# Optimization experiments

Measured on AMD Instinct MI355X. Metric: run time of the kernel, lower is better.

## Reference

```python
import jax, jax.numpy as jnp
import numpy as np

B, S, H = 2, 2048, 2048
NH, NKV, HD = 16, 4, 128
SCALING = HD ** -0.5


def rotate_half(x):
    x1, x2 = jnp.split(x, 2, axis=-1)
    return jnp.concatenate((-x2, x1), axis=-1)


def apply_rope(t, cos, sin):
    # t: [B, nh, S, HD]; cos/sin: [B, S, HD] -> unsqueeze head dim
    c = cos[:, None, :, :]
    s = sin[:, None, :, :]
    return t * c + rotate_half(t) * s


def setup_inputs() -> dict:
    key = jax.random.key(0)
    k1, k2, k3, k4, k5 = jax.random.split(key, 5)
    hidden_states = jax.random.normal(k1, (B, S, H), dtype=jnp.float32)
    # real RoPE tables
    inv_freq = 1.0 / (10000.0 ** (jnp.arange(0, HD, 2, dtype=jnp.float32) / HD))
    pos = jnp.arange(S, dtype=jnp.float32)
    freqs = jnp.einsum('s,d->sd', pos, inv_freq)              # [S, HD/2]
    emb = jnp.concatenate((freqs, freqs), axis=-1)            # [S, HD]
    cos = jnp.broadcast_to(jnp.cos(emb)[None], (B, S, HD))
    sin = jnp.broadcast_to(jnp.sin(emb)[None], (B, S, HD))
    # additive causal mask [B, 1, S, S]
    causal = jnp.triu(jnp.full((S, S), -1e9, dtype=jnp.float32), k=1)
    attention_mask = jnp.broadcast_to(causal[None, None], (B, 1, S, S))
    sc = 0.02
    wq = jax.random.normal(k2, (NH * HD, H), dtype=jnp.float32) * sc
    wk = jax.random.normal(k3, (NKV * HD, H), dtype=jnp.float32) * sc
    wv = jax.random.normal(k4, (NKV * HD, H), dtype=jnp.float32) * sc
    wo = jax.random.normal(k5, (H, NH * HD), dtype=jnp.float32) * sc
    return {"hidden_states": hidden_states, "cos": cos, "sin": sin,
            "attention_mask": attention_mask, "wq": wq, "wk": wk, "wv": wv, "wo": wo}


def reference(hidden_states, cos, sin, attention_mask, wq, wk, wv, wo):
    x = hidden_states
    # fused-style QKV projections (nn.Linear: x @ W.T), split heads -> [B, nh, S, HD]
    q = (x @ wq.T).reshape(B, S, NH, HD).transpose(0, 2, 1, 3)
    k = (x @ wk.T).reshape(B, S, NKV, HD).transpose(0, 2, 1, 3)
    v = (x @ wv.T).reshape(B, S, NKV, HD).transpose(0, 2, 1, 3)
    q = apply_rope(q, cos, sin)
    k = apply_rope(k, cos, sin)
    # GQA: repeat KV heads (repeat_kv)
    n_rep = NH // NKV
    k = jnp.repeat(k, n_rep, axis=1)
    v = jnp.repeat(v, n_rep, axis=1)
    scores = jnp.einsum('bhqd,bhkd->bhqk', q, k) * SCALING + attention_mask
    attn = jax.nn.softmax(scores.astype(jnp.float32), axis=-1).astype(q.dtype)
    out = jnp.einsum('bhqk,bhkd->bhqd', attn, v)
    out = out.transpose(0, 2, 1, 3).reshape(B, S, NH * HD)
    out = out @ wo.T
    return (out, attn)
```

## Files before the change

### kernel.cpp

```cpp
#include <hip/hip_runtime.h>
#include <cstdint>
#include <cstddef>

typedef __bf16 bf16;
typedef __attribute__((ext_vector_type(8))) __bf16 bf16x8;
typedef __attribute__((ext_vector_type(4))) __bf16 bf16x4;
typedef __attribute__((ext_vector_type(4))) float f32x4;

constexpr int B_ = 2, S_ = 2048, H_ = 2048, NH_ = 16, NKV_ = 4, HD_ = 128;
constexpr float SCALE_ = 0.08838834764831845f;

#define GLDS16(g, l)                                                        \
  __builtin_amdgcn_global_load_lds(                                         \
      (const __attribute__((address_space(1))) void*)(g),                   \
      (__attribute__((address_space(3))) void*)(l), 16, 0, 0)

#define VMCNT0 asm volatile("s_waitcnt vmcnt(0)" ::: "memory")
#define VMCNT4 asm volatile("s_waitcnt vmcnt(4)" ::: "memory")
#define BAR __builtin_amdgcn_s_barrier()

__global__ void cvt_all(const float* __restrict__ hs, const float* __restrict__ wq,
                        const float* __restrict__ wk, const float* __restrict__ wv,
                        const float* __restrict__ wo, bf16* __restrict__ xb,
                        bf16* __restrict__ w3b, bf16* __restrict__ wob) {
  const int stride = gridDim.x * blockDim.x;
  for (int i = blockIdx.x * blockDim.x + threadIdx.x; i < 4718592; i += stride) {
    const float4* s; bf16x4* d; int j;
    if (i < 2097152)      { s = (const float4*)hs; d = (bf16x4*)xb;            j = i; }
    else if (i < 3145728) { s = (const float4*)wq; d = (bf16x4*)w3b;           j = i - 2097152; }
    else if (i < 3407872) { s = (const float4*)wk; d = (bf16x4*)w3b + 1048576; j = i - 3145728; }
    else if (i < 3670016) { s = (const float4*)wv; d = (bf16x4*)w3b + 1310720; j = i - 3407872; }
    else                  { s = (const float4*)wo; d = (bf16x4*)wob;           j = i - 3670016; }
    float4 v = s[j];
    bf16x4 o;
    o[0] = (bf16)v.x; o[1] = (bf16)v.y; o[2] = (bf16)v.z; o[3] = (bf16)v.w;
    d[j] = o;
  }
}

template <int EPI>
__global__ __launch_bounds__(256) void gemm_bt(const bf16* __restrict__ A,
                                               const bf16* __restrict__ Bm, int K,
                                               bf16* __restrict__ qb, bf16* __restrict__ kb,
                                               bf16* __restrict__ vtb, float* __restrict__ Cout) {
  __shared__ __align__(16) bf16 As[128 * 64];
  __shared__ __align__(16) bf16 Bs[128 * 64];
  const int tid = threadIdx.x;
  const int lane = tid & 63;
  const int wid = tid >> 6;
  const int fid = blockIdx.y * 32 + blockIdx.x;
  const int nwg = gridDim.y * 32;
  const int swz = (fid & 7) * (nwg >> 3) + (fid >> 3);
  const int m0 = (swz & 31) * 128;
  const int n0 = (swz >> 5) * 128;
  const int wm = (wid >> 1) * 64, wn = (wid & 1) * 64;
  const int r = lane & 15, g = lane >> 4;
  f32x4 acc[4][4] = {};

#pragma unroll 1
  for (int kt = 0; kt < K; kt += 64) {
    __syncthreads();
#pragma unroll
    for (int i = 0; i < 4; ++i) {
      int cb = wid * 256 + i * 64;
      int c64 = cb + lane;
      int row = c64 >> 3, cs = (c64 & 7) ^ (row & 7);
      GLDS16(A + (size_t)(m0 + row) * K + kt + cs * 8, As + cb * 8);
      GLDS16(Bm + (size_t)(n0 + row) * K + kt + cs * 8, Bs + cb * 8);
    }
    VMCNT0;
    __syncthreads();
#pragma unroll
    for (int ks = 0; ks < 2; ++ks) {
      bf16x8 af[4], bfr[4];
#pragma unroll
      for (int fm = 0; fm < 4; ++fm)
        af[fm] = *(const bf16x8*)(As + (wm + fm * 16 + r) * 64 + (((ks * 4 + g) ^ (r & 7)) << 3));
#pragma unroll
      for (int fn = 0; fn < 4; ++fn)
        bfr[fn] = *(const bf16x8*)(Bs + (wn + fn * 16 + r) * 64 + (((ks * 4 + g) ^ (r & 7)) << 3));
#pragma unroll
      for (int fm = 0; fm < 4; ++fm)
#pragma unroll
        for (int fn = 0; fn < 4; ++fn)
          acc[fm][fn] = __builtin_amdgcn_mfma_f32_16x16x32_bf16(af[fm], bfr[fn], acc[fm][fn], 0, 0, 0);
    }
  }

#pragma unroll
  for (int fm = 0; fm < 4; ++fm)
#pragma unroll
    for (int fn = 0; fn < 4; ++fn)
#pragma unroll
      for (int rr = 0; rr < 4; ++rr) {
        int mm = m0 + wm + fm * 16 + g * 4 + rr;
        int nn = n0 + wn + fn * 16 + r;
        float v = acc[fm][fn][rr];
        if (EPI == 1) {
          Cout[(size_t)mm * 2048 + nn] = v;
        } else {
          int b = mm >> 11, s = mm & (S_ - 1);
          int d = nn & 127;
          if (nn < 2048) {
            int hh = nn >> 7;
            qb[(((size_t)b * NH_ + hh) * S_ + s) * HD_ + d] = (bf16)v;
          } else if (nn < 2560) {
            int hh = (nn - 2048) >> 7;
            kb[(((size_t)b * NKV_ + hh) * S_ + s) * HD_ + d] = (bf16)v;
          } else {
            int hh = (nn - 2560) >> 7;
            vtb[(((size_t)b * NKV_ + hh) * HD_ + d) * S_ + s] = (bf16)v;
          }
        }
      }
}

__global__ void rope_k_kernel(bf16* __restrict__ kb, const float* __restrict__ cosp,
                              const float* __restrict__ sinp) {
  const int NK = B_ * NKV_ * S_;
  int t = blockIdx.x * blockDim.x + threadIdx.x;
  if (t >= NK * 8) return;
  const int oct = t & 7, rid = t >> 3;
  bf16* base = kb + (size_t)rid * HD_;
  const int s = rid & (S_ - 1);
  const int b = rid >> 13;
  const int d = oct * 8;
  const float* cp = cosp + ((size_t)b * S_ + s) * HD_ + d;
  const float* sp = sinp + ((size_t)b * S_ + s) * HD_ + d;
  float4 c0 = *(const float4*)cp, c1 = *(const float4*)(cp + 4);
  float4 s0 = *(const float4*)sp, s1 = *(const float4*)(sp + 4);
  float cc[8] = {c0.x, c0.y, c0.z, c0.w, c1.x, c1.y, c1.z, c1.w};
  float ss[8] = {s0.x, s0.y, s0.z, s0.w, s1.x, s1.y, s1.z, s1.w};
  bf16x8 x1 = *(const bf16x8*)(base + d);
  bf16x8 x2 = *(const bf16x8*)(base + d + 64);
  bf16x8 o1, o2;
#pragma unroll
  for (int i = 0; i < 8; ++i) {
    float a = (float)x1[i], bb = (float)x2[i];
    o1[i] = (bf16)(a * cc[i] - bb * ss[i]);
    o2[i] = (bf16)(bb * cc[i] + a * ss[i]);
  }
  *(bf16x8*)(base + d) = o1;
  *(bf16x8*)(base + d + 64) = o2;
}

__global__ __launch_bounds__(256, 2) void attn_kernel(const bf16* __restrict__ qb,
                                                      const bf16* __restrict__ kb,
                                                      const bf16* __restrict__ vtb,
                                                      const float* __restrict__ cosp,
                                                      const float* __restrict__ sinp,
                                                      bf16* __restrict__ aob,
                                                      float* __restrict__ attn_out) {
  __shared__ __align__(16) bf16 Ks[2][64 * 128];
  __shared__ __align__(16) bf16 Vs[2][128 * 64];
  __shared__ __align__(16) bf16 Ps[64 * 64];
  const int bid = (blockIdx.x & 7) * 64 + (blockIdx.x >> 3);
  const int p = bid & 15;
  const int h = (bid >> 4) & 15;
  const int b = bid >> 8;
  const int kh = h >> 2;
  const int tid = threadIdx.x, lane = tid & 63, wid = tid >> 6;
  const int r = lane & 15, g = lane >> 4;

  const bf16* kbase = kb + ((size_t)b * NKV_ + kh) * S_ * HD_;
  const bf16* vbase = vtb + ((size_t)b * NKV_ + kh) * (size_t)HD_ * S_;
  const size_t ahead = (size_t)(b * NH_ + h) * S_;

  auto stageK = [&](int kt, int cc) {
#pragma unroll
    for (int i = 0; i < 4; ++i) {
      int base = i * 256 + wid * 64;
      int idx = base + lane;
      int row = idx >> 4, ch = (idx & 15) ^ (row & 7);
      GLDS16(kbase + (size_t)(kt * 64 + row) * HD_ + ch * 8, &Ks[cc][base * 8]);
    }
  };
  auto stageV = [&](int kt, int cc) {
#pragma unroll
    for (int i = 0; i < 4; ++i) {
      int base = i * 256 + wid * 64;
      int idx = base + lane;
      int row = idx >> 3, ch = (idx & 7) ^ (row & 7);
      GLDS16(vbase + (size_t)row * S_ + kt * 64 + ch * 8, &Vs[cc][base * 8]);
    }
  };

  int zc = 0;

#pragma unroll 1
  for (int sbi = 0; sbi < 2; ++sbi) {
    const int qt = sbi ? 31 - p : p;
    const int q0 = qt * 64;
    const int nt = qt + 1;
    const bf16* qsrc = qb + ((size_t)(b * NH_ + h) * S_ + q0) * HD_;

    bf16x8 qreg[4];
    {
      const int srow = q0 + wid * 16 + r;
#pragma unroll
      for (int ks = 0; ks < 4; ++ks)
        qreg[ks] = *(const bf16x8*)(qsrc + (wid * 16 + r) * HD_ + ks * 32 + g * 8);
      const float* cp = cosp + ((size_t)b * S_ + srow) * HD_;
      const float* sp = sinp + ((size_t)b * S_ + srow) * HD_;
#pragma unroll
      for (int hf = 0; hf < 2; ++hf) {
        const int d0 = hf * 32 + g * 8;
        float4 ca = *(const float4*)(cp + d0), cb2 = *(const float4*)(cp + d0 + 4);
        float4 sa = *(const float4*)(sp + d0), sb2 = *(const float4*)(sp + d0 + 4);
        float cc[8] = {ca.x, ca.y, ca.z, ca.w, cb2.x, cb2.y, cb2.z, cb2.w};
        float ss[8] = {sa.x, sa.y, sa.z, sa.w, sb2.x, sb2.y, sb2.z, sb2.w};
        bf16x8 lo = qreg[hf], hi = qreg[hf + 2];
#pragma unroll
        for (int i = 0; i < 8; ++i) {
          float a = (float)lo[i], bb = (float)hi[i];
          qreg[hf][i] = (bf16)(a * cc[i] - bb * ss[i]);
          qreg[hf + 2][i] = (bf16)(bb * cc[i] + a * ss[i]);
        }
      }
    }

    float lsum = 0.f;
    stageK(0, 0);
    VMCNT0; BAR;
    int c = 0;
#pragma unroll 1
    for (int kt = 0; kt < nt; ++kt) {
      if (kt + 1 < nt) stageK(kt + 1, c ^ 1);
      const bool dz = (zc <= 30);
      if (dz) {
        int qtz, ktz;
        if (zc < 31 - p) { qtz = p; ktz = p + 1 + zc; }
        else             { qtz = 31 - p; ktz = zc + 1; }
        float* zdst = attn_out + (ahead + qtz * 64) * S_ + ktz * 64;
        float4 z = {0.f, 0.f, 0.f, 0.f};
#pragma unroll
        for (int i = 0; i < 4; ++i) {
          int idx = i * 256 + tid;
          *(float4*)(zdst + (size_t)(idx >> 4) * S_ + (idx & 15) * 4) = z;
        }
        ++zc;
      }
      f32x4 sacc[4] = {};
      __builtin_amdgcn_s_setprio(1);
#pragma unroll
      for (int ks = 0; ks < 4; ++ks)
#pragma unroll
        for (int fn = 0; fn < 4; ++fn) {
          bf16x8 kk = *(const bf16x8*)(&Ks[c][(fn * 16 + r) * 128 + (((ks * 4 + g) ^ (r & 7)) << 3)]);
          sacc[fn] = __builtin_amdgcn_mfma_f32_16x16x32_bf16(kk, qreg[ks], sacc[fn], 0, 0, 0);
        }
      __builtin_amdgcn_s_setprio(0);
      float ts = 0.f;
      if (kt == nt - 1) {
#pragma unroll
        for (int fn = 0; fn < 4; ++fn)
#pragma unroll
          for (int rr = 0; rr < 4; ++rr) {
            bool msk = (fn * 16 + g * 4 + rr) > (wid * 16 + r);
            ts += msk ? 0.f : __expf(sacc[fn][rr] * SCALE_);
          }
      } else {
#pragma unroll
        for (int fn = 0; fn < 4; ++fn)
#pragma unroll
          for (int rr = 0; rr < 4; ++rr) ts += __expf(sacc[fn][rr] * SCALE_);
      }
      ts += __shfl_xor(ts, 16);
      ts += __shfl_xor(ts, 32);
      lsum += ts;
      if (dz) { VMCNT4; } else { VMCNT0; }
      BAR;
      c ^= 1;
    }
    const float rl = 1.0f / lsum;

    f32x4 oacc[8] = {};
    const size_t arow0 = (ahead + q0) * S_;
    stageK(0, 0);
    stageV(0, 0);
    VMCNT0; BAR;
    c = 0;
#pragma unroll 1
    for (int kt = 0; kt < nt; ++kt) {
      if (kt + 1 < nt) { stageK(kt + 1, c ^ 1); stageV(kt + 1, c ^ 1); }
      const int k0 = kt * 64;
      f32x4 sacc[4] = {};
      __builtin_amdgcn_s_setprio(1);
#pragma unroll
      for (int ks = 0; ks < 4; ++ks)
#pragma unroll
        for (int fn = 0; fn < 4; ++fn) {
          bf16x8 kk = *(const bf16x8*)(&Ks[c][(fn * 16 + r) * 128 + (((ks * 4 + g) ^ (r & 7)) << 3)]);
          sacc[fn] = __builtin_amdgcn_mfma_f32_16x16x32_bf16(kk, qreg[ks], sacc[fn], 0, 0, 0);
        }
      __builtin_amdgcn_s_setprio(0);
      const int prow = (wid * 16 + r) * 64;
      if (kt == nt - 1) {
#pragma unroll
        for (int fn = 0; fn < 4; ++fn) {
          bf16x4 pk;
#pragma unroll
          for (int rr = 0; rr < 4; ++rr) {
            bool msk = (fn * 16 + g * 4 + rr) > (wid * 16 + r);
            pk[rr] = (bf16)(msk ? 0.f : __expf(sacc[fn][rr] * SCALE_) * rl);
          }
          *(bf16x4*)(&Ps[prow + ((((fn << 1) | (g >> 1)) ^ (r & 7)) << 3) + ((g & 1) << 2)]) = pk;
        }
      } else {
#pragma unroll
        for (int fn = 0; fn < 4; ++fn) {
          bf16x4 pk;
#pragma unroll
          for (int rr = 0; rr < 4; ++rr)
            pk[rr] = (bf16)(__expf(sacc[fn][rr] * SCALE_) * rl);
          *(bf16x4*)(&Ps[prow + ((((fn << 1) | (g >> 1)) ^ (r & 7)) << 3) + ((g & 1) << 2)]) = pk;
        }
      }
      {
        const int trow = tid >> 2, tcb = (tid & 3) * 16;
        float* dst = attn_out + arow0 + (size_t)trow * S_ + k0 + tcb;
        int ch0 = (tid & 3) * 2;
        bf16x8 p0 = *(const bf16x8*)(&Ps[trow * 64 + ((ch0 ^ (trow & 7)) << 3)]);
        bf16x8 p1 = *(const bf16x8*)(&Ps[trow * 64 + (((ch0 + 1) ^ (trow & 7)) << 3)]);
        float4 o0 = {(float)p0[0], (float)p0[1], (float)p0[2], (float)p0[3]};
        float4 o1 = {(float)p0[4], (float)p0[5], (float)p0[6], (float)p0[7]};
        float4 o2 = {(float)p1[0], (float)p1[1], (float)p1[2], (float)p1[3]};
        float4 o3 = {(float)p1[4], (float)p1[5], (float)p1[6], (float)p1[7]};
        *(float4*)(dst) = o0;
        *(float4*)(dst + 4) = o1;
        *(float4*)(dst + 8) = o2;
        *(float4*)(dst + 12) = o3;
      }
      __builtin_amdgcn_s_setprio(1);
#pragma unroll
      for (int ks = 0; ks < 2; ++ks) {
        bf16x8 pa = *(const bf16x8*)(&Ps[prow + (((ks * 4 + g) ^ (r & 7)) << 3)]);
#pragma unroll
        for (int fn = 0; fn < 8; ++fn) {
          bf16x8 vv = *(const bf16x8*)(&Vs[c][(fn * 16 + r) * 64 + (((ks * 4 + g) ^ (r & 7)) << 3)]);
          oacc[fn] = __builtin_amdgcn_mfma_f32_16x16x32_bf16(pa, vv, oacc[fn], 0, 0, 0);
        }
      }
      __builtin_amdgcn_s_setprio(0);
      VMCNT4; BAR;
      c ^= 1;
    }

#pragma unroll
    for (int fn = 0; fn < 8; ++fn)
#pragma unroll
      for (int rr = 0; rr < 4; ++rr) {
        int q = q0 + wid * 16 + g * 4 + rr;
        aob[((size_t)b * S_ + q) * 2048 + h * HD_ + fn * 16 + r] = (bf16)oacc[fn][rr];
      }
  }
}

extern "C" void kernel_launch(void* const* d_in, const int* in_sizes, int n_in,
                              void* d_out, int out_size, void* d_ws, size_t ws_size,
                              hipStream_t stream) {
  const float* hidden = (const float*)d_in[0];
  const float* cosp = (const float*)d_in[1];
  const float* sinp = (const float*)d_in[2];
  const float* wq = (const float*)d_in[4];
  const float* wk = (const float*)d_in[5];
  const float* wv = (const float*)d_in[6];
  const float* wo = (const float*)d_in[7];
  float* out = (float*)d_out;
  float* attn = out + (size_t)B_ * S_ * H_;

  char* ws = (char*)d_ws;
  bf16* xb  = (bf16*)(ws);
  bf16* w3b = (bf16*)(ws + (16ull << 20));
  bf16* wob = (bf16*)(ws + (28ull << 20));
  bf16* qb  = (bf16*)(ws + (36ull << 20));
  bf16* kb  = (bf16*)(ws + (52ull << 20));
  bf16* vtb = (bf16*)(ws + (56ull << 20));
  bf16* aob = (bf16*)(ws + (60ull << 20));

  cvt_all<<<2048, 256, 0, stream>>>(hidden, wq, wk, wv, wo, xb, w3b, wob);
  gemm_bt<0><<<dim3(32, 24), 256, 0, stream>>>(xb, w3b, 2048, qb, kb, vtb, nullptr);
  rope_k_kernel<<<512, 256, 0, stream>>>(kb, cosp, sinp);
  attn_kernel<<<512, 256, 0, stream>>>(qb, kb, vtb, cosp, sinp, aob, attn);
  gemm_bt<1><<<dim3(32, 16), 256, 0, stream>>>(aob, wob, 2048, nullptr, nullptr, nullptr, out);
}
```

Baseline: 347.8 us.

## Single-buffer K/V tiles for higher occupancy and store probabilities from registers

Replaces the double-buffered K/V LDS staging with single buffers loaded synchronously each iteration, fenced by syncthreads. This shrinks shared memory per block, and launch bounds are raised to allow 4 blocks per CU. The attention-probability output is now written as fp32 directly from the MFMA accumulator registers instead of being read back from the bf16 Ps tile. The aim is more occupancy and less LDS traffic, but it gives up load/compute overlap, writes to global memory in a more scattered pattern, and may tighten the register budget. With only 512 blocks in the grid, the extra occupancy may not help.

```diff
diff --git a/kernel.cpp b/kernel.cpp
--- a/kernel.cpp
+++ b/kernel.cpp
@@ -16,7 +16,6 @@
       (__attribute__((address_space(3))) void*)(l), 16, 0, 0)
 
 #define VMCNT0 asm volatile("s_waitcnt vmcnt(0)" ::: "memory")
-#define VMCNT4 asm volatile("s_waitcnt vmcnt(4)" ::: "memory")
 #define BAR __builtin_amdgcn_s_barrier()
 
 __global__ void cvt_all(const float* __restrict__ hs, const float* __restrict__ wq,
@@ -144,15 +143,15 @@
   *(bf16x8*)(base + d + 64) = o2;
 }
 
-__global__ __launch_bounds__(256, 2) void attn_kernel(const bf16* __restrict__ qb,
+__global__ __launch_bounds__(256, 4) void attn_kernel(const bf16* __restrict__ qb,
                                                       const bf16* __restrict__ kb,
                                                       const bf16* __restrict__ vtb,
                                                       const float* __restrict__ cosp,
                                                       const float* __restrict__ sinp,
                                                       bf16* __restrict__ aob,
                                                       float* __restrict__ attn_out) {
-  __shared__ __align__(16) bf16 Ks[2][64 * 128];
-  __shared__ __align__(16) bf16 Vs[2][128 * 64];
+  __shared__ __align__(16) bf16 Ks[64 * 128];
+  __shared__ __align__(16) bf16 Vs[128 * 64];
   __shared__ __align__(16) bf16 Ps[64 * 64];
   const int bid = (blockIdx.x & 7) * 64 + (blockIdx.x >> 3);
   const int p = bid & 15;
@@ -166,22 +165,22 @@
   const bf16* vbase = vtb + ((size_t)b * NKV_ + kh) * (size_t)HD_ * S_;
   const size_t ahead = (size_t)(b * NH_ + h) * S_;
 
-  auto stageK = [&](int kt, int cc) {
+  auto stageK = [&](int kt) {
 #pragma unroll
     for (int i = 0; i < 4; ++i) {
       int base = i * 256 + wid * 64;
       int idx = base + lane;
       int row = idx >> 4, ch = (idx & 15) ^ (row & 7);
-      GLDS16(kbase + (size_t)(kt * 64 + row) * HD_ + ch * 8, &Ks[cc][base * 8]);
+      GLDS16(kbase + (size_t)(kt * 64 + row) * HD_ + ch * 8, Ks + base * 8);
     }
   };
-  auto stageV = [&](int kt, int cc) {
+  auto stageV = [&](int kt) {
 #pragma unroll
     for (int i = 0; i < 4; ++i) {
       int base = i * 256 + wid * 64;
       int idx = base + lane;
       int row = idx >> 3, ch = (idx & 7) ^ (row & 7);
-      GLDS16(vbase + (size_t)row * S_ + kt * 64 + ch * 8, &Vs[cc][base * 8]);
+      GLDS16(vbase + (size_t)row * S_ + kt * 64 + ch * 8, Vs + base * 8);
     }
   };
 
@@ -220,14 +219,13 @@
     }
 
     float lsum = 0.f;
-    stageK(0, 0);
-    VMCNT0; BAR;
-    int c = 0;
 #pragma unroll 1
     for (int kt = 0; kt < nt; ++kt) {
-      if (kt + 1 < nt) stageK(kt + 1, c ^ 1);
-      const bool dz = (zc <= 30);
-      if (dz) {
+      __syncthreads();
+      stageK(kt);
+      VMCNT0;
+      __syncthreads();
+      if (zc <= 30) {
         int qtz, ktz;
         if (zc < 31 - p) { qtz = p; ktz = p + 1 + zc; }
         else             { qtz = 31 - p; ktz = zc + 1; }
@@ -246,7 +244,7 @@
       for (int ks = 0; ks < 4; ++ks)
 #pragma unroll
         for (int fn = 0; fn < 4; ++fn) {
-          bf16x8 kk = *(const bf16x8*)(&Ks[c][(fn * 16 + r) * 128 + (((ks * 4 + g) ^ (r & 7)) << 3)]);
+          bf16x8 kk = *(const bf16x8*)(Ks + (fn * 16 + r) * 128 + (((ks * 4 + g) ^ (r & 7)) << 3));
           sacc[fn] = __builtin_amdgcn_mfma_f32_16x16x32_bf16(kk, qreg[ks], sacc[fn], 0, 0, 0);
         }
       __builtin_amdgcn_s_setprio(0);
@@ -268,68 +266,44 @@
       ts += __shfl_xor(ts, 16);
       ts += __shfl_xor(ts, 32);
       lsum += ts;
-      if (dz) { VMCNT4; } else { VMCNT0; }
-      BAR;
-      c ^= 1;
     }
     const float rl = 1.0f / lsum;
 
     f32x4 oacc[8] = {};
     const size_t arow0 = (ahead + q0) * S_;
-    stageK(0, 0);
-    stageV(0, 0);
-    VMCNT0; BAR;
-    c = 0;
 #pragma unroll 1
     for (int kt = 0; kt < nt; ++kt) {
-      if (kt + 1 < nt) { stageK(kt + 1, c ^ 1); stageV(kt + 1, c ^ 1); }
       const int k0 = kt * 64;
+      __syncthreads();
+      stageK(kt);
+      stageV(kt);
+      VMCNT0;
+      __syncthreads();
       f32x4 sacc[4] = {};
       __builtin_amdgcn_s_setprio(1);
 #pragma unroll
       for (int ks = 0; ks < 4; ++ks)
 #pragma unroll
         for (int fn = 0; fn < 4; ++fn) {
-          bf16x8 kk = *(const bf16x8*)(&Ks[c][(fn * 16 + r) * 128 + (((ks * 4 + g) ^ (r & 7)) << 3)]);
+          bf16x8 kk = *(const bf16x8*)(Ks + (fn * 16 + r) * 128 + (((ks * 4 + g) ^ (r & 7)) << 3));
           sacc[fn] = __builtin_amdgcn_mfma_f32_16x16x32_bf16(kk, qreg[ks], sacc[fn], 0, 0, 0);
         }
       __builtin_amdgcn_s_setprio(0);
       const int prow = (wid * 16 + r) * 64;
-      if (kt == nt - 1) {
-#pragma unroll
-        for (int fn = 0; fn < 4; ++fn) {
-          bf16x4 pk;
-#pragma unroll
-          for (int rr = 0; rr < 4; ++rr) {
-            bool msk = (fn * 16 + g * 4 + rr) > (wid * 16 + r);
-            pk[rr] = (bf16)(msk ? 0.f : __expf(sacc[fn][rr] * SCALE_) * rl);
-          }
-          *(bf16x4*)(&Ps[prow + ((((fn << 1) | (g >> 1)) ^ (r & 7)) << 3) + ((g & 1) << 2)]) = pk;
-        }
-      } else {
-#pragma unroll
-        for (int fn = 0; fn < 4; ++fn) {
-          bf16x4 pk;
-#pragma unroll
-          for (int rr = 0; rr < 4; ++rr)
-            pk[rr] = (bf16)(__expf(sacc[fn][rr] * SCALE_) * rl);
-          *(bf16x4*)(&Ps[prow + ((((fn << 1) | (g >> 1)) ^ (r & 7)) << 3) + ((g & 1) << 2)]) = pk;
-        }
-      }
-      {
-        const int trow = tid >> 2, tcb = (tid & 3) * 16;
-        float* dst = attn_out + arow0 + (size_t)trow * S_ + k0 + tcb;
-        int ch0 = (tid & 3) * 2;
-        bf16x8 p0 = *(const bf16x8*)(&Ps[trow * 64 + ((ch0 ^ (trow & 7)) << 3)]);
-        bf16x8 p1 = *(const bf16x8*)(&Ps[trow * 64 + (((ch0 + 1) ^ (trow & 7)) << 3)]);
-        float4 o0 = {(float)p0[0], (float)p0[1], (float)p0[2], (float)p0[3]};
-        float4 o1 = {(float)p0[4], (float)p0[5], (float)p0[6], (float)p0[7]};
-        float4 o2 = {(float)p1[0], (float)p1[1], (float)p1[2], (float)p1[3]};
-        float4 o3 = {(float)p1[4], (float)p1[5], (float)p1[6], (float)p1[7]};
-        *(float4*)(dst) = o0;
-        *(float4*)(dst + 4) = o1;
-        *(float4*)(dst + 8) = o2;
-        *(float4*)(dst + 12) = o3;
+      const bool last = (kt == nt - 1);
+#pragma unroll
+      for (int fn = 0; fn < 4; ++fn) {
+        float4 pv4;
+        bf16x4 pk;
+#pragma unroll
+        for (int rr = 0; rr < 4; ++rr) {
+          bool msk = last && ((fn * 16 + g * 4 + rr) > (wid * 16 + r));
+          float f = msk ? 0.f : __expf(sacc[fn][rr] * SCALE_) * rl;
+          ((float*)&pv4)[rr] = f;
+          pk[rr] = (bf16)f;
+        }
+        *(float4*)(attn_out + arow0 + (size_t)(wid * 16 + r) * S_ + k0 + fn * 16 + g * 4) = pv4;
+        *(bf16x4*)(&Ps[prow + ((((fn << 1) | (g >> 1)) ^ (r & 7)) << 3) + ((g & 1) << 2)]) = pk;
       }
       __builtin_amdgcn_s_setprio(1);
 #pragma unroll
@@ -337,13 +311,11 @@
         bf16x8 pa = *(const bf16x8*)(&Ps[prow + (((ks * 4 + g) ^ (r & 7)) << 3)]);
 #pragma unroll
         for (int fn = 0; fn < 8; ++fn) {
-          bf16x8 vv = *(const bf16x8*)(&Vs[c][(fn * 16 + r) * 64 + (((ks * 4 + g) ^ (r & 7)) << 3)]);
+          bf16x8 vv = *(const bf16x8*)(Vs + (fn * 16 + r) * 64 + (((ks * 4 + g) ^ (r & 7)) << 3));
           oacc[fn] = __builtin_amdgcn_mfma_f32_16x16x32_bf16(pa, vv, oacc[fn], 0, 0, 0);
         }
       }
       __builtin_amdgcn_s_setprio(0);
-      VMCNT4; BAR;
-      c ^= 1;
     }
 
 #pragma unroll
```

New measurement: 350.1 us. About the same (+0.7%).
